# Kernel tuning notes

Measured on AMD Instinct MI355X. Metric: run time of the kernel, lower is better.

Reference implementation:

```python
import jax, jax.numpy as jnp
import numpy as np

GROUPS = 32
EPS = 1e-5


def setup_inputs() -> dict:
    key = jax.random.key(0)
    ks = jax.random.split(key, 4)
    b, c, h, w = 4, 256, 64, 64
    x = jax.random.normal(ks[0], (b, c, h, w), dtype=jnp.float32)
    gn_gamma = jnp.ones((c,), dtype=jnp.float32)
    gn_beta = jnp.zeros((c,), dtype=jnp.float32)
    # 1x1 convs are pointwise linear maps: store kernels as [out, in]
    w_qkv = jax.random.normal(ks[1], (3 * c, c), dtype=jnp.float32) * (1.0 / np.sqrt(c))
    b_qkv = jnp.zeros((3 * c,), dtype=jnp.float32)
    w_out = jax.random.normal(ks[2], (c, c), dtype=jnp.float32) * (1.0 / np.sqrt(c))
    b_out = jnp.zeros((c,), dtype=jnp.float32)
    return {"x": x, "gn_gamma": gn_gamma, "gn_beta": gn_beta,
            "w_qkv": w_qkv, "b_qkv": b_qkv, "w_out": w_out, "b_out": b_out}


def reference(x, gn_gamma, gn_beta, w_qkv, b_qkv, w_out, b_out):
    b, c, h, w = x.shape
    # GroupNorm(32, c)
    xg = x.reshape(b, GROUPS, c // GROUPS, h, w)
    mean = jnp.mean(xg, axis=(2, 3, 4), keepdims=True)
    var = jnp.var(xg, axis=(2, 3, 4), keepdims=True)
    xn = ((xg - mean) * jax.lax.rsqrt(var + EPS)).reshape(b, c, h, w)
    xn = xn * gn_gamma[None, :, None, None] + gn_beta[None, :, None, None]
    # 1x1 conv QKV projection: [b, 3c, h, w]
    qkv = jnp.einsum('bchw,oc->bohw', xn, w_qkv) + b_qkv[None, :, None, None]
    q, k, v = jnp.split(qkv, 3, axis=1)
    n = h * w
    q = q.transpose(0, 2, 3, 1).reshape(b, n, c)  # [b, n, c]
    k = k.reshape(b, c, n)                        # [b, c, n]
    v = v.transpose(0, 2, 3, 1).reshape(b, n, c)  # [b, n, c]
    scores = jnp.einsum('bic,bcj->bij', q, k) * (c ** -0.5)  # [b, n, n]
    attn = jax.nn.softmax(scores, axis=-1)
    out = jnp.einsum('bij,bjc->bic', attn, v)     # [b, n, c]
    out = out.reshape(b, h, w, c).transpose(0, 3, 1, 2)  # [b, c, h, w]
    out = jnp.einsum('bchw,oc->bohw', out, w_out) + b_out[None, :, None, None]
    return out + x
```

## Files before the change

kernel.cpp:

```cpp
#include <hip/hip_runtime.h>
#include <hip/hip_bf16.h>
#include <cstdint>
#include <cstddef>

#define DEVINL __device__ __forceinline__

typedef unsigned short u16;
typedef unsigned char u8;
typedef unsigned int u32;
typedef unsigned long long u64;
typedef __attribute__((ext_vector_type(8))) short short8;
typedef __attribute__((ext_vector_type(4))) float f32x4;
typedef __attribute__((ext_vector_type(4))) u16 u16x4;

constexpr int CH = 256;
constexpr int HW = 4096;
constexpr int NB = 4;
constexpr float M0L = 5.7707801636f;
constexpr float QKS = 0.3002805f;

DEVINL u16 f2bf(float f) {
  union { float f; u32 u; } v; v.f = f;
  u32 u = v.u;
  u32 r = u + 0x7FFFu + ((u >> 16) & 1u);
  return (u16)(r >> 16);
}
DEVINL float bf2f(u16 h) {
  union { u32 u; float f; } v; v.u = ((u32)h) << 16; return v.f;
}
DEVINL float fexp2(float x) {
  float r; asm("v_exp_f32 %0, %1" : "=v"(r) : "v"(x)); return r;
}
DEVINL u8 f2fp8(float v) {
  return (u8)(__builtin_amdgcn_cvt_pk_fp8_f32(v, v, 0, false) & 0xFF);
}
DEVINL u32 pk4fp8(float v0, float v1, float v2, float v3) {
  int r = __builtin_amdgcn_cvt_pk_fp8_f32(v0, v1, 0, false);
  r = __builtin_amdgcn_cvt_pk_fp8_f32(v2, v3, r, true);
  return (u32)r;
}
DEVINL void plswap(u32& a, u32& b) {
  asm("v_permlane32_swap_b32 %0, %1" : "+v"(a), "+v"(b));
  asm("v_permlane16_swap_b32 %0, %1" : "+v"(a), "+v"(b));
}

DEVINL void gl_lds16(const void* g, void* l) {
  __builtin_amdgcn_global_load_lds(
      (__attribute__((address_space(1))) void*)(size_t)g,
      (__attribute__((address_space(3))) void*)l, 16, 0, 0);
}

DEVINL f32x4 mfma_bf16(short8 a, short8 b, f32x4 c) {
  return __builtin_amdgcn_mfma_f32_16x16x32_bf16(a, b, c, 0, 0, 0);
}
DEVINL f32x4 mfma_fp8(long a, long b, f32x4 c) {
  return __builtin_amdgcn_mfma_f32_16x16x32_fp8_fp8(a, b, c, 0, 0, 0);
}

__global__ void k_pre(const float* __restrict__ x, float* __restrict__ stats,
                      const float* __restrict__ wq, const float* __restrict__ wo,
                      u8* __restrict__ w38, u16* __restrict__ wob) {
  if (blockIdx.x >= 128) {
    int i = (blockIdx.x - 128) * 256 + threadIdx.x;
    w38[i] = f2fp8(wq[i]);
    if (i < 65536) wob[i] = f2bf(wo[i]);
    return;
  }
  int bg = blockIdx.x;
  const float* p = x + (size_t)bg * 32768;
  float s = 0.f, ss = 0.f;
  for (int i = threadIdx.x; i < 8192; i += 256) {
    float4 v = ((const float4*)p)[i];
    s += v.x + v.y + v.z + v.w;
    ss += v.x * v.x + v.y * v.y + v.z * v.z + v.w * v.w;
  }
  for (int m = 32; m; m >>= 1) { s += __shfl_xor(s, m); ss += __shfl_xor(ss, m); }
  __shared__ float rs[4], rss[4];
  int w = threadIdx.x >> 6;
  if ((threadIdx.x & 63) == 0) { rs[w] = s; rss[w] = ss; }
  __syncthreads();
  if (threadIdx.x == 0) {
    s = rs[0] + rs[1] + rs[2] + rs[3];
    ss = rss[0] + rss[1] + rss[2] + rss[3];
    float mean = s / 32768.f;
    float var = ss / 32768.f - mean * mean;
    stats[bg * 2] = mean;
    stats[bg * 2 + 1] = rsqrtf(var + 1e-5f);
  }
}

__global__ void k_norm(const float* __restrict__ x, const float* __restrict__ stats,
                       const float* __restrict__ gamma, const float* __restrict__ beta,
                       u8* __restrict__ xn8) {
  int bid = blockIdx.x;
  int b = bid >> 8, ct = (bid >> 6) & 3, pt = bid & 63;
  int c0 = ct * 64, p0 = pt * 64;
  __shared__ u16 tile[64][66];
  const float* xb = x + ((size_t)b * CH + c0) * HW + p0;
#pragma unroll
  for (int it = 0; it < 4; it++) {
    int li = threadIdx.x + it * 256;
    int ci = li >> 4, pq = (li & 15) * 4;
    float4 v = *(const float4*)(xb + (size_t)ci * HW + pq);
    int c = c0 + ci;
    int gg = c >> 3;
    float mean = stats[(b * 32 + gg) * 2], rstd = stats[(b * 32 + gg) * 2 + 1];
    float ga = gamma[c] * rstd;
    float be = beta[c] - mean * ga;
    tile[ci][pq + 0] = f2bf(v.x * ga + be);
    tile[ci][pq + 1] = f2bf(v.y * ga + be);
    tile[ci][pq + 2] = f2bf(v.z * ga + be);
    tile[ci][pq + 3] = f2bf(v.w * ga + be);
  }
  __syncthreads();
#pragma unroll
  for (int it = 0; it < 2; it++) {
    int ch = threadIdx.x + it * 256;
    int pr = ch >> 3, cc = (ch & 7) * 8;
    float v[8];
#pragma unroll
    for (int q2 = 0; q2 < 8; q2++) v[q2] = bf2f(tile[cc + q2][pr]);
    u32 lo = pk4fp8(v[0], v[1], v[2], v[3]);
    u32 hi = pk4fp8(v[4], v[5], v[6], v[7]);
    *(u64*)(xn8 + ((size_t)b * HW + p0 + pr) * CH + c0 + cc) = ((u64)hi << 32) | lo;
  }
}

DEVINL void stage_tile(char* dst, const u16* src_rows, int kt, int w, int lane) {
#pragma unroll
  for (int it = 0; it < 4; it++) {
    int CI = w * 256 + it * 64 + lane;
    int row = CI >> 3, ci = CI & 7;
    int sci = ci ^ (row & 7);
    gl_lds16(src_rows + (size_t)row * 256 + kt * 64 + sci * 8,
             dst + w * 4096 + it * 1024);
  }
}

DEVINL short8 ldsA(const char* base, int row, int colb) {
  return *(const short8*)(base + row * 128 + (colb ^ ((row & 7) << 4)));
}

__global__ __launch_bounds__(256, 2) void k_qkv(
    const u8* __restrict__ xn8, const u8* __restrict__ w38,
    const float* __restrict__ bqkv,
    u8* __restrict__ Qg8, u8* __restrict__ Kg8, u8* __restrict__ Vg8) {
  int bid = blockIdx.x;
  int b = bid / 192; int rm = bid - b * 192; int mt = rm / 6, nt = rm - mt * 6;
  extern __shared__ char sm[];
  const int tid = threadIdx.x, w = tid >> 6, lane = tid & 63, t = lane & 15, g = lane >> 4;
  const u8* Abase = xn8 + ((size_t)b * HW + mt * 128) * CH;
  const u8* Bbase = w38 + (size_t)nt * 128 * CH;
  f32x4 acc[4][4] = {};

  auto stg = [&](char* dst, const u8* src, int kt) {
#pragma unroll
    for (int it = 0; it < 2; it++) {
      int CI = w * 128 + it * 64 + lane;
      int row = CI >> 2, c4 = CI & 3;
      int sc = c4 ^ ((row ^ (row >> 2)) & 3);
      gl_lds16(src + (size_t)row * CH + kt * 64 + sc * 16, dst + w * 2048 + it * 1024);
    }
  };

  stg(sm, Abase, 0);
  stg(sm + 16384, Bbase, 0);
  __syncthreads();
  for (int kt = 0; kt < 4; kt++) {
    int cur = kt & 1;
    if (kt < 3) {
      stg(sm + ((cur ^ 1) * 8192), Abase, kt + 1);
      stg(sm + 16384 + ((cur ^ 1) * 8192), Bbase, kt + 1);
    }
    const char* Asm = sm + cur * 8192;
    const char* Bsm = sm + 16384 + cur * 8192;
#pragma unroll
    for (int ks = 0; ks < 2; ks++) {
      long af[4], bf4[4];
#pragma unroll
      for (int m = 0; m < 4; m++) {
        int r = 64 * (w >> 1) + 16 * m + t;
        af[m] = *(const long*)(Asm + r * 64 +
                 (((ks * 2 + (g >> 1)) ^ ((r ^ (r >> 2)) & 3)) << 4) + ((g & 1) << 3));
      }
#pragma unroll
      for (int n = 0; n < 4; n++) {
        int r = 64 * (w & 1) + 16 * n + t;
        bf4[n] = *(const long*)(Bsm + r * 64 +
                 (((ks * 2 + (g >> 1)) ^ ((r ^ (r >> 2)) & 3)) << 4) + ((g & 1) << 3));
      }
#pragma unroll
      for (int m = 0; m < 4; m++)
#pragma unroll
        for (int n = 0; n < 4; n++)
          acc[m][n] = mfma_fp8(af[m], bf4[n], acc[m][n]);
    }
    __syncthreads();
  }
#pragma unroll
  for (int n = 0; n < 4; n++) {
    int o = nt * 128 + 64 * (w & 1) + 16 * n + t;
    float bias = bqkv[o];
#pragma unroll
    for (int m = 0; m < 4; m++) {
      int p0 = mt * 128 + 64 * (w >> 1) + 16 * m + 4 * g;
      if (nt < 4) {
        u8* dst = (nt < 2) ? Qg8 : Kg8;
        int oo = (nt < 2) ? o : o - 256;
#pragma unroll
        for (int rr = 0; rr < 4; rr++) {
          float v = (acc[m][n][rr] + bias) * QKS;
          dst[((size_t)b * HW + p0 + rr) * CH + oo] = f2fp8(v);
        }
      } else {
        int oo = o - 512;
        u32 pv = pk4fp8(acc[m][n][0] + bias, acc[m][n][1] + bias,
                        acc[m][n][2] + bias, acc[m][n][3] + bias);
        *(u32*)(Vg8 + (size_t)b * CH * HW + (size_t)oo * HW + p0) = pv;
      }
    }
  }
}

__global__ __launch_bounds__(512, 2) void k_attn(
    const u8* __restrict__ Qg8, const u8* __restrict__ Kg8, const u8* __restrict__ Vg8,
    u8* __restrict__ Op8, float* __restrict__ ml) {
  int bid = blockIdx.x;
  int qb = bid >> 4, b = (bid >> 2) & 3, split = bid & 3;
  extern __shared__ char sm[];
  const int tid = threadIdx.x, w = tid >> 6, lane = tid & 63, t = lane & 15, g = lane >> 4;
  const u8* Qb = Qg8 + (size_t)b * HW * CH;
  const u8* Kb = Kg8 + (size_t)b * HW * CH;
  const u8* Vb = Vg8 + (size_t)b * CH * HW;
  int qrow0 = qb * 256 + w * 32;
  int kv0 = split * 1024;

  long q8[2][8];
#pragma unroll
  for (int rf = 0; rf < 2; rf++)
#pragma unroll
    for (int ks = 0; ks < 8; ks++)
      q8[rf][ks] = *(const long*)(Qb + (size_t)(qrow0 + rf * 16 + t) * CH + ks * 32 + g * 8);

  f32x4 oacc[2][16] = {};
  float lsum[2] = {0.f, 0.f};
  f32x4 sf[2][4];
  long pf[2][2];

  int kOffB[2], vOffB[2];
#pragma unroll
  for (int it = 0; it < 2; it++) {
    int CI = w * 128 + it * 64 + lane;
    int row = CI >> 4, c = CI & 15;
    kOffB[it] = row * 256 + ((c ^ (row & 7)) * 16);
    int rv = CI >> 2, c4 = CI & 3;
    vOffB[it] = rv * HW + ((c4 ^ ((rv >> 1) & 3)) * 16);
  }
  auto stageKV = [&](int kbuf, int vbuf, int tt) {
    char* KL = sm + kbuf * 16384 + w * 2048;
    char* VL = sm + 49152 + vbuf * 16384 + w * 2048;
    const u8* ksrc = Kb + (size_t)(kv0 + tt * 64) * CH;
    const u8* vsrc = Vb + (kv0 + tt * 64);
#pragma unroll
    for (int it = 0; it < 2; it++) gl_lds16(ksrc + kOffB[it], KL + it * 1024);
#pragma unroll
    for (int it = 0; it < 2; it++) gl_lds16(vsrc + vOffB[it], VL + it * 1024);
  };

  auto QK = [&](const char* KL) {
#pragma unroll
    for (int jf = 0; jf < 4; jf++) {
      int row = jf * 16 + t;
      f32x4 a0 = {}, a1 = {};
#pragma unroll
      for (int ks = 0; ks < 8; ks++) {
        int s = ks * 4 + g;
        long kf = *(const long*)(KL + row * 256 + (((s >> 1) ^ (row & 7)) << 4) + ((s & 1) << 3));
        a0 = mfma_fp8(kf, q8[0][ks], a0);
        a1 = mfma_fp8(kf, q8[1][ks], a1);
      }
      sf[0][jf] = a0; sf[1][jf] = a1;
    }
  };
  auto PV = [&](const char* VL) {
#pragma unroll
    for (int ks = 0; ks < 2; ks++)
#pragma unroll
      for (int cf = 0; cf < 16; cf++) {
        int row = cf * 16 + t;
        long vf = *(const long*)(VL + row * 64 +
                    (((ks * 2 + (g >> 1)) ^ ((row >> 1) & 3)) << 4) + ((g & 1) << 3));
        oacc[0][cf] = mfma_fp8(pf[0][ks], vf, oacc[0][cf]);
        oacc[1][cf] = mfma_fp8(pf[1][ks], vf, oacc[1][cf]);
      }
  };
  auto SM = [&]() {
#pragma unroll
    for (int rf = 0; rf < 2; rf++) {
      u32 A4[4];
#pragma unroll
      for (int jf = 0; jf < 4; jf++) {
        float e0 = fexp2(sf[rf][jf][0] - M0L);
        float e1 = fexp2(sf[rf][jf][1] - M0L);
        float e2 = fexp2(sf[rf][jf][2] - M0L);
        float e3 = fexp2(sf[rf][jf][3] - M0L);
        lsum[rf] += (e0 + e1) + (e2 + e3);
        A4[jf] = pk4fp8(e0, e1, e2, e3);
      }
#pragma unroll
      for (int ks = 0; ks < 2; ks++) {
        u32 X = A4[2 * ks], Y = A4[2 * ks + 1];
        plswap(X, Y);
        pf[rf][ks] = (long)(((u64)Y << 32) | X);
      }
    }
  };

  stageKV(0, 0, 0);
  stageKV(1, 1, 1);
  asm volatile("s_waitcnt vmcnt(4)" ::: "memory");
  __builtin_amdgcn_s_barrier();
  __builtin_amdgcn_sched_barrier(0);
  __builtin_amdgcn_s_setprio(1);
  QK(sm + 0);
  __builtin_amdgcn_s_setprio(0);
  SM();

  for (int tt = 1; tt < 16; tt++) {
    int kcur = tt % 3, vprv = (tt - 1) & 3;
    stageKV((tt + 1) % 3, (tt + 1) & 3, (tt + 1) & 15);
    asm volatile("s_waitcnt vmcnt(4)" ::: "memory");
    __builtin_amdgcn_s_barrier();
    __builtin_amdgcn_sched_barrier(0);
    __builtin_amdgcn_s_setprio(1);
    PV(sm + 49152 + vprv * 16384);
    QK(sm + kcur * 16384);
    __builtin_amdgcn_s_setprio(0);
    SM();
  }
  __builtin_amdgcn_s_setprio(1);
  PV(sm + 49152 + 3 * 16384);
  __builtin_amdgcn_s_setprio(0);

  size_t obase = (size_t)(split * NB + b) * HW;
#pragma unroll
  for (int rf = 0; rf < 2; rf++) {
    float ls = lsum[rf];
    ls += __shfl_xor(ls, 16);
    ls += __shfl_xor(ls, 32);
    if (g == 0) ml[obase + qrow0 + rf * 16 + t] = ls;
    float invr[4];
#pragma unroll
    for (int rr = 0; rr < 4; rr++) invr[rr] = 1.f / __shfl(ls, 4 * g + rr);
#pragma unroll
    for (int cf = 0; cf < 16; cf++)
#pragma unroll
      for (int rr = 0; rr < 4; rr++) {
        int row = qrow0 + rf * 16 + 4 * g + rr;
        Op8[(obase + row) * CH + cf * 16 + t] = f2fp8(oacc[rf][cf][rr] * invr[rr]);
      }
  }
}

__global__ __launch_bounds__(256, 1) void k_oproj(
    const u16* __restrict__ wob, const u8* __restrict__ Op8, const float* __restrict__ ml,
    const float* __restrict__ bout, const float* __restrict__ x,
    float* __restrict__ out) {
  int bid = blockIdx.x;
  int b = bid >> 6, pt = bid & 63;
  extern __shared__ char sm[];
  const int tid = threadIdx.x, w = tid >> 6, lane = tid & 63, t = lane & 15, g = lane >> 4;

  auto stageA = [&](char* dst, int kt) {
#pragma unroll
    for (int it = 0; it < 8; it++) {
      int CI = w * 512 + it * 64 + lane;
      int row = CI >> 3, ci = CI & 7;
      int sci = ci ^ (row & 7);
      gl_lds16(wob + (size_t)row * CH + kt * 64 + sci * 8,
               dst + w * 8192 + it * 1024);
    }
  };
  auto stageB = [&](char* dst, int kt) {
#pragma unroll
    for (int it = 0; it < 2; it++) {
      int CI = w * 128 + it * 64 + lane;
      int row = CI >> 3, ci = CI & 7;
      int sci = ci ^ (row & 7);
      int p = pt * 64 + row;
      float l = 0.f;
      float accv[8] = {};
#pragma unroll
      for (int s = 0; s < 4; s++) {
        size_t r = (size_t)(s * NB + b) * HW + p;
        float lsv = ml[r];
        l += lsv;
        u64 a8 = *(const u64*)(Op8 + r * CH + kt * 64 + sci * 8);
        u32 wlo = (u32)a8, whi = (u32)(a8 >> 32);
        accv[0] += lsv * __builtin_amdgcn_cvt_f32_fp8(wlo, 0);
        accv[1] += lsv * __builtin_amdgcn_cvt_f32_fp8(wlo, 1);
        accv[2] += lsv * __builtin_amdgcn_cvt_f32_fp8(wlo, 2);
        accv[3] += lsv * __builtin_amdgcn_cvt_f32_fp8(wlo, 3);
        accv[4] += lsv * __builtin_amdgcn_cvt_f32_fp8(whi, 0);
        accv[5] += lsv * __builtin_amdgcn_cvt_f32_fp8(whi, 1);
        accv[6] += lsv * __builtin_amdgcn_cvt_f32_fp8(whi, 2);
        accv[7] += lsv * __builtin_amdgcn_cvt_f32_fp8(whi, 3);
      }
      float inv = 1.f / l;
      short8 res;
#pragma unroll
      for (int q2 = 0; q2 < 8; q2++) res[q2] = (short)f2bf(accv[q2] * inv);
      *(short8*)(dst + CI * 16) = res;
    }
  };

  f32x4 acc[4][4] = {};
  stageA(sm, 0);
  stageB(sm + 65536, 0);
  __syncthreads();
  for (int kt = 0; kt < 4; kt++) {
    int cur = kt & 1;
    if (kt < 3) {
      stageA(sm + ((cur ^ 1) * 32768), kt + 1);
      stageB(sm + 65536 + ((cur ^ 1) * 8192), kt + 1);
    }
    const char* Asm = sm + cur * 32768;
    const char* Bsm = sm + 65536 + cur * 8192;
#pragma unroll
    for (int ks = 0; ks < 2; ks++) {
      short8 af[4], bf[4];
#pragma unroll
      for (int m = 0; m < 4; m++) af[m] = ldsA(Asm, w * 64 + 16 * m + t, ks * 64 + g * 16);
#pragma unroll
      for (int n = 0; n < 4; n++) bf[n] = ldsA(Bsm, 16 * n + t, ks * 64 + g * 16);
#pragma unroll
      for (int m = 0; m < 4; m++)
#pragma unroll
        for (int n = 0; n < 4; n++)
          acc[m][n] = mfma_bf16(af[m], bf[n], acc[m][n]);
    }
    __syncthreads();
  }
#pragma unroll
  for (int m = 0; m < 4; m++) {
    int o0 = w * 64 + 16 * m + 4 * g;
#pragma unroll
    for (int n = 0; n < 4; n++) {
      int p = pt * 64 + 16 * n + t;
#pragma unroll
      for (int rr = 0; rr < 4; rr++) {
        int o = o0 + rr;
        size_t off = ((size_t)b * CH + o) * HW + p;
        out[off] = acc[m][n][rr] + bout[o] + x[off];
      }
    }
  }
}

extern "C" void kernel_launch(void* const* d_in, const int* in_sizes, int n_in,
                              void* d_out, int out_size, void* d_ws, size_t ws_size,
                              hipStream_t stream) {
  const float* x = (const float*)d_in[0];
  const float* gamma = (const float*)d_in[1];
  const float* beta = (const float*)d_in[2];
  const float* wqkv = (const float*)d_in[3];
  const float* bqkv = (const float*)d_in[4];
  const float* wout = (const float*)d_in[5];
  const float* bout = (const float*)d_in[6];
  float* out = (float*)d_out;
  char* ws = (char*)d_ws;

  float* stats = (float*)(ws);
  u8* w38 = (u8*)(ws + 1024);
  u16* wob = (u16*)(ws + 1024 + 196608);
  u8* xn8 = (u8*)(ws + 1024 + 196608 + 131072);
  u8* Qg8 = (u8*)(ws + 328704 + 1ull * 4194304);
  u8* Kg8 = (u8*)(ws + 328704 + 2ull * 4194304);
  u8* Vg8 = (u8*)(ws + 328704 + 3ull * 4194304);
  u8* Op8 = (u8*)(ws + 328704 + 4ull * 4194304);
  float* ml = (float*)(ws + 328704 + 8ull * 4194304);

  hipFuncSetAttribute(reinterpret_cast<const void*>(k_qkv),
                      hipFuncAttributeMaxDynamicSharedMemorySize, 32768);
  hipFuncSetAttribute(reinterpret_cast<const void*>(k_oproj),
                      hipFuncAttributeMaxDynamicSharedMemorySize, 81920);
  hipFuncSetAttribute(reinterpret_cast<const void*>(k_attn),
                      hipFuncAttributeMaxDynamicSharedMemorySize, 114688);

  k_pre<<<896, 256, 0, stream>>>(x, stats, wqkv, wout, w38, wob);
  k_norm<<<1024, 256, 0, stream>>>(x, stats, gamma, beta, xn8);
  k_qkv<<<768, 256, 32768, stream>>>(xn8, w38, bqkv, Qg8, Kg8, Vg8);
  k_attn<<<256, 512, 114688, stream>>>(Qg8, Kg8, Vg8, Op8, ml);
  k_oproj<<<256, 256, 81920, stream>>>(wob, Op8, ml, bout, x, out);
}
```

Measured before the change: 102.1 us.

## Permute channel layout so Q/K and attention outputs store as packed words

```diff
diff --git a/kernel.cpp b/kernel.cpp
--- a/kernel.cpp
+++ b/kernel.cpp
@@ -11,7 +11,7 @@
 typedef unsigned long long u64;
 typedef __attribute__((ext_vector_type(8))) short short8;
 typedef __attribute__((ext_vector_type(4))) float f32x4;
-typedef __attribute__((ext_vector_type(4))) u16 u16x4;
+typedef __attribute__((ext_vector_type(4))) u32 u32x4;
 
 constexpr int CH = 256;
 constexpr int HW = 4096;
@@ -57,13 +57,17 @@
   return __builtin_amdgcn_mfma_f32_16x16x32_fp8_fp8(a, b, c, 0, 0, 0);
 }
 
+
 __global__ void k_pre(const float* __restrict__ x, float* __restrict__ stats,
                       const float* __restrict__ wq, const float* __restrict__ wo,
-                      u8* __restrict__ w38, u16* __restrict__ wob) {
+                      u8* __restrict__ w38, u16* __restrict__ wobP) {
   if (blockIdx.x >= 128) {
     int i = (blockIdx.x - 128) * 256 + threadIdx.x;
     w38[i] = f2fp8(wq[i]);
-    if (i < 65536) wob[i] = f2bf(wo[i]);
+    if (i < 65536) {
+      int o = i >> 8, pc = i & 255;
+      wobP[i] = f2bf(wo[o * 256 + ((pc & 15) * 16 + (pc >> 4))]);
+    }
     return;
   }
   int bg = blockIdx.x;
@@ -126,17 +130,6 @@
   }
 }
 
-DEVINL void stage_tile(char* dst, const u16* src_rows, int kt, int w, int lane) {
-#pragma unroll
-  for (int it = 0; it < 4; it++) {
-    int CI = w * 256 + it * 64 + lane;
-    int row = CI >> 3, ci = CI & 7;
-    int sci = ci ^ (row & 7);
-    gl_lds16(src_rows + (size_t)row * 256 + kt * 64 + sci * 8,
-             dst + w * 4096 + it * 1024);
-  }
-}
-
 DEVINL short8 ldsA(const char* base, int row, int colb) {
   return *(const short8*)(base + row * 128 + (colb ^ ((row & 7) << 4)));
 }
@@ -197,23 +190,33 @@
     }
     __syncthreads();
   }
-#pragma unroll
-  for (int n = 0; n < 4; n++) {
-    int o = nt * 128 + 64 * (w & 1) + 16 * n + t;
-    float bias = bqkv[o];
+  if (nt < 4) {
+    u8* dst = (nt < 2) ? Qg8 : Kg8;
+    int pcb = t * 16 + (nt & 1) * 8 + 4 * (w & 1);
+    float bias[4];
+#pragma unroll
+    for (int n = 0; n < 4; n++) bias[n] = bqkv[nt * 128 + 64 * (w & 1) + 16 * n + t];
 #pragma unroll
     for (int m = 0; m < 4; m++) {
       int p0 = mt * 128 + 64 * (w >> 1) + 16 * m + 4 * g;
-      if (nt < 4) {
-        u8* dst = (nt < 2) ? Qg8 : Kg8;
-        int oo = (nt < 2) ? o : o - 256;
-#pragma unroll
-        for (int rr = 0; rr < 4; rr++) {
-          float v = (acc[m][n][rr] + bias) * QKS;
-          dst[((size_t)b * HW + p0 + rr) * CH + oo] = f2fp8(v);
-        }
-      } else {
-        int oo = o - 512;
+#pragma unroll
+      for (int rr = 0; rr < 4; rr++) {
+        u32 word = pk4fp8((acc[m][0][rr] + bias[0]) * QKS,
+                          (acc[m][1][rr] + bias[1]) * QKS,
+                          (acc[m][2][rr] + bias[2]) * QKS,
+                          (acc[m][3][rr] + bias[3]) * QKS);
+        *(u32*)(dst + ((size_t)b * HW + p0 + rr) * CH + pcb) = word;
+      }
+    }
+  } else {
+#pragma unroll
+    for (int n = 0; n < 4; n++) {
+      int o = nt * 128 + 64 * (w & 1) + 16 * n + t;
+      float bias = bqkv[o];
+      int oo = o - 512;
+#pragma unroll
+      for (int m = 0; m < 4; m++) {
+        int p0 = mt * 128 + 64 * (w >> 1) + 16 * m + 4 * g;
         u32 pv = pk4fp8(acc[m][n][0] + bias, acc[m][n][1] + bias,
                         acc[m][n][2] + bias, acc[m][n][3] + bias);
         *(u32*)(Vg8 + (size_t)b * CH * HW + (size_t)oo * HW + p0) = pv;
@@ -353,17 +356,22 @@
 #pragma unroll
     for (int rr = 0; rr < 4; rr++) invr[rr] = 1.f / __shfl(ls, 4 * g + rr);
 #pragma unroll
-    for (int cf = 0; cf < 16; cf++)
-#pragma unroll
-      for (int rr = 0; rr < 4; rr++) {
-        int row = qrow0 + rf * 16 + 4 * g + rr;
-        Op8[(obase + row) * CH + cf * 16 + t] = f2fp8(oacc[rf][cf][rr] * invr[rr]);
-      }
+    for (int rr = 0; rr < 4; rr++) {
+      int row = qrow0 + rf * 16 + 4 * g + rr;
+      u32x4 wv;
+#pragma unroll
+      for (int q4 = 0; q4 < 4; q4++)
+        wv[q4] = pk4fp8(oacc[rf][4 * q4 + 0][rr] * invr[rr],
+                        oacc[rf][4 * q4 + 1][rr] * invr[rr],
+                        oacc[rf][4 * q4 + 2][rr] * invr[rr],
+                        oacc[rf][4 * q4 + 3][rr] * invr[rr]);
+      *(u32x4*)(Op8 + (obase + row) * CH + t * 16) = wv;
+    }
   }
 }
 
 __global__ __launch_bounds__(256, 1) void k_oproj(
-    const u16* __restrict__ wob, const u8* __restrict__ Op8, const float* __restrict__ ml,
+    const u16* __restrict__ wobP, const u8* __restrict__ Op8, const float* __restrict__ ml,
     const float* __restrict__ bout, const float* __restrict__ x,
     float* __restrict__ out) {
   int bid = blockIdx.x;
@@ -377,7 +385,7 @@
       int CI = w * 512 + it * 64 + lane;
       int row = CI >> 3, ci = CI & 7;
       int sci = ci ^ (row & 7);
-      gl_lds16(wob + (size_t)row * CH + kt * 64 + sci * 8,
+      gl_lds16(wobP + (size_t)row * CH + kt * 64 + sci * 8,
                dst + w * 8192 + it * 1024);
     }
   };
@@ -472,7 +480,7 @@
 
   float* stats = (float*)(ws);
   u8* w38 = (u8*)(ws + 1024);
-  u16* wob = (u16*)(ws + 1024 + 196608);
+  u16* wobP = (u16*)(ws + 1024 + 196608);
   u8* xn8 = (u8*)(ws + 1024 + 196608 + 131072);
   u8* Qg8 = (u8*)(ws + 328704 + 1ull * 4194304);
   u8* Kg8 = (u8*)(ws + 328704 + 2ull * 4194304);
@@ -487,9 +495,9 @@
   hipFuncSetAttribute(reinterpret_cast<const void*>(k_attn),
                       hipFuncAttributeMaxDynamicSharedMemorySize, 114688);
 
-  k_pre<<<896, 256, 0, stream>>>(x, stats, wqkv, wout, w38, wob);
+  k_pre<<<896, 256, 0, stream>>>(x, stats, wqkv, wout, w38, wobP);
   k_norm<<<1024, 256, 0, stream>>>(x, stats, gamma, beta, xn8);
   k_qkv<<<768, 256, 32768, stream>>>(xn8, w38, bqkv, Qg8, Kg8, Vg8);
   k_attn<<<256, 512, 114688, stream>>>(Qg8, Kg8, Vg8, Op8, ml);
-  k_oproj<<<256, 256, 81920, stream>>>(wob, Op8, ml, bout, x, out);
-}
+  k_oproj<<<256, 256, 81920, stream>>>(wobP, Op8, ml, bout, x, out);
+}
```

New measurement: 99.81 us. 1.02x faster.
